# Kernel optimization log

Hardware: AMD Instinct MI355X
Metric: run time of the kernel (lower is better)

Reference implementation:

```python
import jax, jax.numpy as jnp
import numpy as np

D = 256  # out_size / d_model
B, S = 8, 4096


def setup_inputs() -> dict:
    key = jax.random.key(0)
    ks = jax.random.split(key, 10)
    std = 1.0 / np.sqrt(D)
    x = jax.random.normal(ks[0], (B, S, D), dtype=jnp.float32)
    Wq = jax.random.uniform(ks[1], (D, D), jnp.float32, -std, std)
    bq = jax.random.uniform(ks[2], (D,), jnp.float32, -std, std)
    Wk = jax.random.uniform(ks[3], (D, D), jnp.float32, -std, std)
    bk = jax.random.uniform(ks[4], (D,), jnp.float32, -std, std)
    Wv = jax.random.uniform(ks[5], (D, D), jnp.float32, -std, std)
    bv = jax.random.uniform(ks[6], (D,), jnp.float32, -std, std)
    Wo = jax.random.uniform(ks[7], (D, D), jnp.float32, -std, std)
    bo = jax.random.uniform(ks[8], (D,), jnp.float32, -std, std)
    cv = jax.random.normal(ks[9], (D, 1), dtype=jnp.float32)
    return {"x": x, "Wq": Wq, "bq": bq, "Wk": Wk, "bk": bk,
            "Wv": Wv, "bv": bv, "Wo": Wo, "bo": bo, "cv": cv}


def reference(x, Wq, bq, Wk, bk, Wv, bv, Wo, bo, cv):
    # Local single-head attention: separate matmul / softmax / matmul
    q = jnp.einsum('bsd,de->bse', x, Wq) + bq
    k = jnp.einsum('bsd,de->bse', x, Wk) + bk
    v = jnp.einsum('bsd,de->bse', x, Wv) + bv
    scale = jnp.sqrt(jnp.asarray(D, dtype=x.dtype))
    scores = jnp.einsum('bqd,bkd->bqk', q, k) / scale  # [B,S,S]
    attn = jax.nn.softmax(scores, axis=-1)
    ctx = jnp.einsum('bqk,bkd->bqd', attn, v)
    logits = jnp.einsum('bsd,de->bse', ctx, Wo) + bo
    # Global context-vector pooling weights (softmax over sequence dim)
    w = jnp.einsum('bsd,dk->bsk', logits, cv)          # [B,S,1]
    nw = jax.nn.softmax(w, axis=1)
    return logits * nw
```

## Files before the change

### kernel.cpp

```cpp
#include <hip/hip_runtime.h>
#include <math.h>
#include <cstddef>
#include <cstdint>

#define B_ 8
#define S_ 4096
#define D_ 256

typedef __attribute__((ext_vector_type(8))) short short8v;
typedef __attribute__((ext_vector_type(4))) short short4v;
typedef __attribute__((ext_vector_type(4))) float float4v;

__device__ __forceinline__ unsigned short f2bf(float f) {
  unsigned u = __float_as_uint(f);
  return (unsigned short)((u + 0x7FFF + ((u >> 16) & 1)) >> 16);
}
__device__ __forceinline__ float bf2f(unsigned short h) {
  return __uint_as_float((unsigned)h << 16);
}
__device__ __forceinline__ unsigned packp(float p) {
  const unsigned short hh = f2bf(p);
  const unsigned short ll = f2bf(p - bf2f(hh));
  return ((unsigned)hh << 16) | (unsigned)ll;
}

__global__ __launch_bounds__(256) void wsplit_kernel(
    const float* __restrict__ Wq, const float* __restrict__ Wk,
    const float* __restrict__ Wv, const float* __restrict__ Wo,
    short* __restrict__ wsp) {
  const int mat = blockIdx.x >> 4;
  const int k0  = (blockIdx.x & 15) << 4;
  const float* W = (mat == 0) ? Wq : (mat == 1) ? Wk : (mat == 2) ? Wv : Wo;
  const int n = threadIdx.x;
  short8v h0, h1, l0, l1;
#pragma unroll
  for (int j = 0; j < 8; ++j) {
    float y = W[(size_t)(k0 + j) * 256 + n];
    unsigned short hh = f2bf(y);
    h0[j] = (short)hh; l0[j] = (short)f2bf(y - bf2f(hh));
    y = W[(size_t)(k0 + 8 + j) * 256 + n];
    hh = f2bf(y);
    h1[j] = (short)hh; l1[j] = (short)f2bf(y - bf2f(hh));
  }
  short* dh = wsp + (size_t)mat * 131072 + (size_t)n * 256 + k0;
  short* dl = dh + 65536;
  *(short8v*)(dh + 0) = h0; *(short8v*)(dh + 8) = h1;
  *(short8v*)(dl + 0) = l0; *(short8v*)(dl + 8) = l1;
}

__global__ __launch_bounds__(512, 2) void proj_qkv_mfma(
    const float* __restrict__ x, const short* __restrict__ wsp,
    const float* __restrict__ bq, const float* __restrict__ bk,
    const float* __restrict__ bvv,
    short* __restrict__ qh, short* __restrict__ ql,
    short* __restrict__ kh, short* __restrict__ kl,
    short* __restrict__ vth, short* __restrict__ vtl) {
  __shared__ __align__(16) short sWh[256 * 40];
  __shared__ __align__(16) short sWl[256 * 40];

  const int t    = threadIdx.x;
  const int w    = t >> 6;
  const int lane = t & 63;
  const int m    = lane & 15;
  const int quad = lane >> 4;
  const size_t r0 = (size_t)blockIdx.x * 128;
  const size_t srow = r0 + 16 * w + m;

  short8v xh[8], xl[8];
#pragma unroll
  for (int kk = 0; kk < 8; ++kk) {
    const float* xp = x + srow * 256 + kk * 32 + quad * 8;
    const float4 a = *(const float4*)xp;
    const float4 b2 = *(const float4*)(xp + 4);
    const float v[8] = {a.x, a.y, a.z, a.w, b2.x, b2.y, b2.z, b2.w};
    short8v h, l;
#pragma unroll
    for (int e = 0; e < 8; ++e) {
      const unsigned short hh = f2bf(v[e]);
      h[e] = (short)hh; l[e] = (short)f2bf(v[e] - bf2f(hh));
    }
    xh[kk] = h; xl[kk] = l;
  }

  const int nr   = t >> 1;
  const int kh16 = (t & 1) << 4;
  short8v rh0, rh1, rl0, rl1;
  {
    const short* gh = wsp + (size_t)nr * 256 + kh16;
    const short* gl = gh + 65536;
    rh0 = *(const short8v*)gh;       rh1 = *(const short8v*)(gh + 8);
    rl0 = *(const short8v*)gl;       rl1 = *(const short8v*)(gl + 8);
  }

#pragma unroll
  for (int p = 0; p < 3; ++p) {
    float4v acc[16];
#pragma unroll
    for (int nt = 0; nt < 16; ++nt) acc[nt] = (float4v){0.f, 0.f, 0.f, 0.f};

    for (int kk = 0; kk < 8; ++kk) {
      asm volatile("s_waitcnt lgkmcnt(0)" ::: "memory");
      __builtin_amdgcn_s_barrier();
      asm volatile("" ::: "memory");
      *(short8v*)&sWh[nr * 40 + kh16]     = rh0;
      *(short8v*)&sWh[nr * 40 + kh16 + 8] = rh1;
      *(short8v*)&sWl[nr * 40 + kh16]     = rl0;
      *(short8v*)&sWl[nr * 40 + kh16 + 8] = rl1;
      {
        const int np = (kk < 7) ? p : p + 1;
        const int nk = (kk < 7) ? kk + 1 : 0;
        if (np < 3) {
          const short* gh = wsp + (size_t)np * 131072 +
                            (size_t)nr * 256 + nk * 32 + kh16;
          const short* gl = gh + 65536;
          rh0 = *(const short8v*)gh;   rh1 = *(const short8v*)(gh + 8);
          rl0 = *(const short8v*)gl;   rl1 = *(const short8v*)(gl + 8);
        }
      }
      asm volatile("s_waitcnt lgkmcnt(0)" ::: "memory");
      __builtin_amdgcn_s_barrier();
      asm volatile("" ::: "memory");

      __builtin_amdgcn_s_setprio(1);
#pragma unroll
      for (int nt = 0; nt < 16; ++nt) {
        const short8v wh = *(const short8v*)&sWh[(nt * 16 + m) * 40 + quad * 8];
        const short8v wl = *(const short8v*)&sWl[(nt * 16 + m) * 40 + quad * 8];
        if (p < 2) {
          acc[nt] = __builtin_amdgcn_mfma_f32_16x16x32_bf16(wh, xh[kk], acc[nt], 0, 0, 0);
          acc[nt] = __builtin_amdgcn_mfma_f32_16x16x32_bf16(wh, xl[kk], acc[nt], 0, 0, 0);
          acc[nt] = __builtin_amdgcn_mfma_f32_16x16x32_bf16(wl, xh[kk], acc[nt], 0, 0, 0);
        } else {
          acc[nt] = __builtin_amdgcn_mfma_f32_16x16x32_bf16(xh[kk], wh, acc[nt], 0, 0, 0);
          acc[nt] = __builtin_amdgcn_mfma_f32_16x16x32_bf16(xh[kk], wl, acc[nt], 0, 0, 0);
          acc[nt] = __builtin_amdgcn_mfma_f32_16x16x32_bf16(xl[kk], wh, acc[nt], 0, 0, 0);
        }
      }
      __builtin_amdgcn_s_setprio(0);
    }

    if (p < 2) {
      const float scale = (p == 0) ? 0.0625f : 1.0f;
      short* oh = (p == 0) ? qh : kh;
      short* ol = (p == 0) ? ql : kl;
      const float* bias = (p == 0) ? bq : bk;
#pragma unroll
      for (int nt = 0; nt < 16; ++nt) {
        const float4 bb = *(const float4*)(bias + nt * 16 + quad * 4);
        const float bb4[4] = {bb.x, bb.y, bb.z, bb.w};
        short4v h4, l4;
#pragma unroll
        for (int r = 0; r < 4; ++r) {
          const float y = (acc[nt][r] + bb4[r]) * scale;
          const unsigned short hh = f2bf(y);
          h4[r] = (short)hh; l4[r] = (short)f2bf(y - bf2f(hh));
        }
        *(short4v*)(oh + srow * 256 + nt * 16 + quad * 4) = h4;
        *(short4v*)(ol + srow * 256 + nt * 16 + quad * 4) = l4;
      }
    } else {
      const int bidx = (int)(r0 >> 12);
      const size_t bD = (size_t)bidx * (D_ * (size_t)S_);
      const int sl0 = (int)(r0 & 4095) + 16 * w + quad * 4;
#pragma unroll
      for (int nt = 0; nt < 16; ++nt) {
        const int d = nt * 16 + m;
        const float bn = bvv[d];
        short4v h4, l4;
#pragma unroll
        for (int r = 0; r < 4; ++r) {
          const float y = acc[nt][r] + bn;
          const unsigned short hh = f2bf(y);
          h4[r] = (short)hh; l4[r] = (short)f2bf(y - bf2f(hh));
        }
        *(short4v*)(vth + bD + (size_t)d * S_ + sl0) = h4;
        *(short4v*)(vtl + bD + (size_t)d * S_ + sl0) = l4;
      }
    }
  }
}

__global__ __launch_bounds__(512, 2) void gemm_out_mfma(
    const float* __restrict__ ctx, const short* __restrict__ wsp,
    const float* __restrict__ bo, const float* __restrict__ cv,
    float* __restrict__ out, float* __restrict__ wvec) {
  __shared__ __align__(16) short sWh[256 * 40];
  __shared__ __align__(16) short sWl[256 * 40];

  const int t    = threadIdx.x;
  const int w    = t >> 6;
  const int lane = t & 63;
  const int m    = lane & 15;
  const int quad = lane >> 4;
  const size_t r0 = (size_t)blockIdx.x * 128;
  const size_t srow = r0 + 16 * w + m;
  const short* wbase = wsp + (size_t)3 * 131072;

  short8v ah[8], al[8];
#pragma unroll
  for (int kk = 0; kk < 8; ++kk) {
    const float* xp = ctx + srow * 256 + kk * 32 + quad * 8;
    const float4 a = *(const float4*)xp;
    const float4 b2 = *(const float4*)(xp + 4);
    const float v[8] = {a.x, a.y, a.z, a.w, b2.x, b2.y, b2.z, b2.w};
    short8v h, l;
#pragma unroll
    for (int e = 0; e < 8; ++e) {
      const unsigned short hh = f2bf(v[e]);
      h[e] = (short)hh; l[e] = (short)f2bf(v[e] - bf2f(hh));
    }
    ah[kk] = h; al[kk] = l;
  }

  const int nr   = t >> 1;
  const int kh16 = (t & 1) << 4;
  short8v rh0, rh1, rl0, rl1;
  {
    const short* gh = wbase + (size_t)nr * 256 + kh16;
    const short* gl = gh + 65536;
    rh0 = *(const short8v*)gh;       rh1 = *(const short8v*)(gh + 8);
    rl0 = *(const short8v*)gl;       rl1 = *(const short8v*)(gl + 8);
  }

  float4v acc[16];
#pragma unroll
  for (int nt = 0; nt < 16; ++nt) acc[nt] = (float4v){0.f, 0.f, 0.f, 0.f};

  for (int kk = 0; kk < 8; ++kk) {
    asm volatile("s_waitcnt lgkmcnt(0)" ::: "memory");
    __builtin_amdgcn_s_barrier();
    asm volatile("" ::: "memory");
    *(short8v*)&sWh[nr * 40 + kh16]     = rh0;
    *(short8v*)&sWh[nr * 40 + kh16 + 8] = rh1;
    *(short8v*)&sWl[nr * 40 + kh16]     = rl0;
    *(short8v*)&sWl[nr * 40 + kh16 + 8] = rl1;
    if (kk < 7) {
      const short* gh = wbase + (size_t)nr * 256 + (kk + 1) * 32 + kh16;
      const short* gl = gh + 65536;
      rh0 = *(const short8v*)gh;   rh1 = *(const short8v*)(gh + 8);
      rl0 = *(const short8v*)gl;   rl1 = *(const short8v*)(gl + 8);
    }
    asm volatile("s_waitcnt lgkmcnt(0)" ::: "memory");
    __builtin_amdgcn_s_barrier();
    asm volatile("" ::: "memory");

    __builtin_amdgcn_s_setprio(1);
#pragma unroll
    for (int nt = 0; nt < 16; ++nt) {
      const short8v wh = *(const short8v*)&sWh[(nt * 16 + m) * 40 + quad * 8];
      const short8v wl = *(const short8v*)&sWl[(nt * 16 + m) * 40 + quad * 8];
      acc[nt] = __builtin_amdgcn_mfma_f32_16x16x32_bf16(wh, ah[kk], acc[nt], 0, 0, 0);
      acc[nt] = __builtin_amdgcn_mfma_f32_16x16x32_bf16(wh, al[kk], acc[nt], 0, 0, 0);
      acc[nt] = __builtin_amdgcn_mfma_f32_16x16x32_bf16(wl, ah[kk], acc[nt], 0, 0, 0);
    }
    __builtin_amdgcn_s_setprio(0);
  }

  float wp = 0.f;
  float* orow = out + srow * 256;
#pragma unroll
  for (int nt = 0; nt < 16; ++nt) {
    const float4 bb = *(const float4*)(bo + nt * 16 + quad * 4);
    const float4 cc = *(const float4*)(cv + nt * 16 + quad * 4);
    float4 o;
    o.x = acc[nt][0] + bb.x; o.y = acc[nt][1] + bb.y;
    o.z = acc[nt][2] + bb.z; o.w = acc[nt][3] + bb.w;
    wp += o.x * cc.x + o.y * cc.y + o.z * cc.z + o.w * cc.w;
    *(float4*)(orow + nt * 16 + quad * 4) = o;
  }
  wp += __shfl_xor(wp, 16, 64);
  wp += __shfl_xor(wp, 32, 64);
  if (quad == 0) wvec[srow] = wp;
}

__global__ __launch_bounds__(512, 2) void flash_attn_mfma(
    const short* __restrict__ qh, const short* __restrict__ ql,
    const short* __restrict__ kh, const short* __restrict__ kl,
    const short* __restrict__ vth, const short* __restrict__ vtl,
    float* __restrict__ ctx) {
  __shared__ __align__(16) short sK[16896];
  __shared__ __align__(16) short sV[20480];
  __shared__ __align__(16) unsigned int sP[8][16][36];
  __shared__ __align__(16) float sAlpha[8][16];
  __shared__ __align__(16) int sF[8];
  __shared__ __align__(16) float sL[128];

  const int t    = threadIdx.x;
  const int w    = t >> 6;
  const int lane = t & 63;
  const int m    = lane & 15;
  const int quad = lane >> 4;
  const int q0   = blockIdx.x * 128;
  const int b    = blockIdx.y;
  const size_t sd = (size_t)b * (S_ * (size_t)D_);
  const size_t bD = (size_t)b * (D_ * (size_t)S_);

  short8v aqh[8], aql[8];
  {
    const size_t row = sd + (size_t)(q0 + 16 * w + m) * D_;
#pragma unroll
    for (int kk = 0; kk < 8; ++kk) {
      const size_t off = row + kk * 32 + quad * 8;
      aqh[kk] = *(const short8v*)(qh + off);
      aql[kk] = *(const short8v*)(ql + off);
    }
  }

  short8v ones;
#pragma unroll
  for (int e = 0; e < 8; ++e) ones[e] = (short)0x3F80;

  float4v acc[8][2];
#pragma unroll
  for (int qt = 0; qt < 8; ++qt) {
    acc[qt][0] = (float4v){0.f, 0.f, 0.f, 0.f};
    acc[qt][1] = (float4v){0.f, 0.f, 0.f, 0.f};
  }
  float4v accl = (float4v){0.f, 0.f, 0.f, 0.f};
  float m_i = -INFINITY;

  const int kr0 = t >> 5;
  const int kc0 = (t & 31) << 3;
  const int vd  = t >> 1;
  const int vjh = (t & 1) << 4;

  short8v rKh0, rKh1, rKl0, rKl1;
  short8v rVh0, rVh1, rVl0, rVl1;

  {
    const size_t g0 = sd + (size_t)kr0 * D_ + kc0;
    const size_t g1 = sd + (size_t)(16 + kr0) * D_ + kc0;
    rKh0 = *(const short8v*)(kh + g0);
    rKh1 = *(const short8v*)(kh + g1);
    rKl0 = *(const short8v*)(kl + g0);
    rKl1 = *(const short8v*)(kl + g1);
  }

  for (int jt = 0; jt < 128; ++jt) {
    const int j0 = jt << 5;

    *(short8v*)&sK[kr0 * 264 + kc0]               = rKh0;
    *(short8v*)&sK[(16 + kr0) * 264 + kc0]        = rKh1;
    *(short8v*)&sK[8448 + kr0 * 264 + kc0]        = rKl0;
    *(short8v*)&sK[8448 + (16 + kr0) * 264 + kc0] = rKl1;
    {
      const size_t g = bD + (size_t)vd * S_ + j0 + vjh;
      rVh0 = *(const short8v*)(vth + g);
      rVh1 = *(const short8v*)(vth + g + 8);
      rVl0 = *(const short8v*)(vtl + g);
      rVl1 = *(const short8v*)(vtl + g + 8);
    }
    asm volatile("s_waitcnt lgkmcnt(0)" ::: "memory");
    __builtin_amdgcn_s_barrier();
    asm volatile("" ::: "memory");

    float4v s0 = (float4v){0.f, 0.f, 0.f, 0.f};
    float4v s1 = (float4v){0.f, 0.f, 0.f, 0.f};
    __builtin_amdgcn_s_setprio(1);
#pragma unroll
    for (int kk = 0; kk < 8; ++kk) {
      const int co = kk * 32 + quad * 8;
      const short8v bh0 = *(const short8v*)&sK[m * 264 + co];
      const short8v bl0 = *(const short8v*)&sK[8448 + m * 264 + co];
      const short8v bh1 = *(const short8v*)&sK[(16 + m) * 264 + co];
      const short8v bl1 = *(const short8v*)&sK[8448 + (16 + m) * 264 + co];
      s0 = __builtin_amdgcn_mfma_f32_16x16x32_bf16(bh0, aqh[kk], s0, 0, 0, 0);
      s0 = __builtin_amdgcn_mfma_f32_16x16x32_bf16(bh0, aql[kk], s0, 0, 0, 0);
      s0 = __builtin_amdgcn_mfma_f32_16x16x32_bf16(bl0, aqh[kk], s0, 0, 0, 0);
      s1 = __builtin_amdgcn_mfma_f32_16x16x32_bf16(bh1, aqh[kk], s1, 0, 0, 0);
      s1 = __builtin_amdgcn_mfma_f32_16x16x32_bf16(bh1, aql[kk], s1, 0, 0, 0);
      s1 = __builtin_amdgcn_mfma_f32_16x16x32_bf16(bl1, aqh[kk], s1, 0, 0, 0);
    }
    __builtin_amdgcn_s_setprio(0);

    float alpha_p = 1.0f;
    int fired = 0;
    {
      float mx = fmaxf(fmaxf(fmaxf(s0[0], s0[1]), fmaxf(s0[2], s0[3])),
                       fmaxf(fmaxf(s1[0], s1[1]), fmaxf(s1[2], s1[3])));
      mx = fmaxf(mx, __shfl_xor(mx, 16, 64));
      mx = fmaxf(mx, __shfl_xor(mx, 32, 64));
      if (__any(mx > m_i + 8.0f)) {
        const float mnew = fmaxf(m_i, mx);
        alpha_p = __expf(m_i - mnew);
        m_i = mnew;
        fired = 1;
        float al[4];
#pragma unroll
        for (int r = 0; r < 4; ++r) al[r] = __shfl(alpha_p, 20 * quad + r, 64);
#pragma unroll
        for (int r = 0; r < 4; ++r) accl[r] *= al[r];
      }
    }
    if (quad == 0) sAlpha[w][m] = alpha_p;
    if (lane == 0) sF[w] = fired;

    {
      uint4 w0, w1;
      w0.x = packp(__expf(s0[0] - m_i));
      w0.y = packp(__expf(s0[1] - m_i));
      w0.z = packp(__expf(s0[2] - m_i));
      w0.w = packp(__expf(s0[3] - m_i));
      w1.x = packp(__expf(s1[0] - m_i));
      w1.y = packp(__expf(s1[1] - m_i));
      w1.z = packp(__expf(s1[2] - m_i));
      w1.w = packp(__expf(s1[3] - m_i));
      *(uint4*)&sP[w][m][4 * quad]      = w0;
      *(uint4*)&sP[w][m][16 + 4 * quad] = w1;
    }

    *(short8v*)&sV[vd * 40 + vjh]               = rVh0;
    *(short8v*)&sV[vd * 40 + vjh + 8]           = rVh1;
    *(short8v*)&sV[10240 + vd * 40 + vjh]       = rVl0;
    *(short8v*)&sV[10240 + vd * 40 + vjh + 8]   = rVl1;
    if (jt < 127) {
      const int j0n = j0 + 32;
      const size_t g0 = sd + (size_t)(j0n + kr0) * D_ + kc0;
      const size_t g1 = sd + (size_t)(j0n + 16 + kr0) * D_ + kc0;
      rKh0 = *(const short8v*)(kh + g0);
      rKh1 = *(const short8v*)(kh + g1);
      rKl0 = *(const short8v*)(kl + g0);
      rKl1 = *(const short8v*)(kl + g1);
    }
    asm volatile("s_waitcnt lgkmcnt(0)" ::: "memory");
    __builtin_amdgcn_s_barrier();
    asm volatile("" ::: "memory");

    {
      const uint4 f0 = *(const uint4*)&sF[0];
      const uint4 f1 = *(const uint4*)&sF[4];
      if (f0.x | f0.y | f0.z | f0.w | f1.x | f1.y | f1.z | f1.w) {
#pragma unroll
        for (int qt = 0; qt < 8; ++qt) {
          const float4 alf = *(const float4*)&sAlpha[qt][quad << 2];
          const float a4[4] = {alf.x, alf.y, alf.z, alf.w};
#pragma unroll
          for (int r = 0; r < 4; ++r) {
            acc[qt][0][r] *= a4[r];
            acc[qt][1][r] *= a4[r];
          }
        }
      }
    }

    __builtin_amdgcn_s_setprio(1);
    {
      const int vr0 = ((w << 1) * 16 + m) * 40 + quad * 8;
      const short8v bh0 = *(const short8v*)&sV[vr0];
      const short8v bl0 = *(const short8v*)&sV[10240 + vr0];
      const short8v bh1 = *(const short8v*)&sV[vr0 + 640];
      const short8v bl1 = *(const short8v*)&sV[10240 + vr0 + 640];
#pragma unroll
      for (int qt = 0; qt < 8; ++qt) {
        short8v ph, pl;
        {
          const uint4 pa = *(const uint4*)&sP[qt][m][quad * 8];
          const uint4 pb = *(const uint4*)&sP[qt][m][quad * 8 + 4];
          ph[0] = (short)(pa.x >> 16); pl[0] = (short)(pa.x & 0xffff);
          ph[1] = (short)(pa.y >> 16); pl[1] = (short)(pa.y & 0xffff);
          ph[2] = (short)(pa.z >> 16); pl[2] = (short)(pa.z & 0xffff);
          ph[3] = (short)(pa.w >> 16); pl[3] = (short)(pa.w & 0xffff);
          ph[4] = (short)(pb.x >> 16); pl[4] = (short)(pb.x & 0xffff);
          ph[5] = (short)(pb.y >> 16); pl[5] = (short)(pb.y & 0xffff);
          ph[6] = (short)(pb.z >> 16); pl[6] = (short)(pb.z & 0xffff);
          ph[7] = (short)(pb.w >> 16); pl[7] = (short)(pb.w & 0xffff);
        }
        if (qt == w) {
          accl = __builtin_amdgcn_mfma_f32_16x16x32_bf16(ph, ones, accl, 0, 0, 0);
          accl = __builtin_amdgcn_mfma_f32_16x16x32_bf16(pl, ones, accl, 0, 0, 0);
        }
        acc[qt][0] = __builtin_amdgcn_mfma_f32_16x16x32_bf16(ph, bh0, acc[qt][0], 0, 0, 0);
        acc[qt][0] = __builtin_amdgcn_mfma_f32_16x16x32_bf16(ph, bl0, acc[qt][0], 0, 0, 0);
        acc[qt][0] = __builtin_amdgcn_mfma_f32_16x16x32_bf16(pl, bh0, acc[qt][0], 0, 0, 0);
        acc[qt][1] = __builtin_amdgcn_mfma_f32_16x16x32_bf16(ph, bh1, acc[qt][1], 0, 0, 0);
        acc[qt][1] = __builtin_amdgcn_mfma_f32_16x16x32_bf16(ph, bl1, acc[qt][1], 0, 0, 0);
        acc[qt][1] = __builtin_amdgcn_mfma_f32_16x16x32_bf16(pl, bh1, acc[qt][1], 0, 0, 0);
      }
    }
    __builtin_amdgcn_s_setprio(0);
  }

  if (m == 0) {
#pragma unroll
    for (int r = 0; r < 4; ++r) sL[16 * w + 4 * quad + r] = accl[r];
  }
  __syncthreads();
#pragma unroll
  for (int qt = 0; qt < 8; ++qt) {
    const float4 lf = *(const float4*)&sL[16 * qt + (quad << 2)];
    const float inv4[4] = {1.0f / lf.x, 1.0f / lf.y, 1.0f / lf.z, 1.0f / lf.w};
#pragma unroll
    for (int dtl = 0; dtl < 2; ++dtl) {
      const int d = ((w << 1) + dtl) * 16 + m;
#pragma unroll
      for (int r = 0; r < 4; ++r) {
        ctx[sd + (size_t)(q0 + 16 * qt + 4 * quad + r) * D_ + d] =
            acc[qt][dtl][r] * inv4[r];
      }
    }
  }
}

__global__ __launch_bounds__(256) void softmax_scale_kernel(
    float* __restrict__ out, const float* __restrict__ wv) {
  __shared__ float red[4];
  const int t = threadIdx.x;
  const int wave = t >> 6, lane = t & 63;
  const int b = blockIdx.x >> 8;
  const float* wb = wv + (size_t)b * S_;

  float mx = -INFINITY;
#pragma unroll
  for (int i = 0; i < 16; ++i) mx = fmaxf(mx, wb[t + (i << 8)]);
#pragma unroll
  for (int off = 32; off > 0; off >>= 1) mx = fmaxf(mx, __shfl_xor(mx, off, 64));
  if (lane == 0) red[wave] = mx;
  __syncthreads();
  const float M = fmaxf(fmaxf(red[0], red[1]), fmaxf(red[2], red[3]));
  float sum = 0.f;
#pragma unroll
  for (int i = 0; i < 16; ++i) sum += __expf(wb[t + (i << 8)] - M);
#pragma unroll
  for (int off = 32; off > 0; off >>= 1) sum += __shfl_xor(sum, off, 64);
  __syncthreads();
  if (lane == 0) red[wave] = sum;
  __syncthreads();
  const float inv = 1.0f / (red[0] + red[1] + red[2] + red[3]);

  float4* o4 = (float4*)out;
  const size_t g0 = (size_t)blockIdx.x * 1024 + t;
#pragma unroll
  for (int i = 0; i < 4; ++i) {
    const size_t g = g0 + (size_t)(i << 8);
    const float sc = __expf(wv[g >> 6] - M) * inv;
    float4 vv = o4[g];
    vv.x *= sc; vv.y *= sc; vv.z *= sc; vv.w *= sc;
    o4[g] = vv;
  }
}

extern "C" void kernel_launch(void* const* d_in, const int* in_sizes, int n_in,
                              void* d_out, int out_size, void* d_ws, size_t ws_size,
                              hipStream_t stream) {
  const float* x  = (const float*)d_in[0];
  const float* Wq = (const float*)d_in[1];
  const float* bq = (const float*)d_in[2];
  const float* Wk = (const float*)d_in[3];
  const float* bk = (const float*)d_in[4];
  const float* Wv = (const float*)d_in[5];
  const float* bv = (const float*)d_in[6];
  const float* Wo = (const float*)d_in[7];
  const float* bo = (const float*)d_in[8];
  const float* cv = (const float*)d_in[9];
  float* out = (float*)d_out;

  const size_t N = (size_t)B_ * S_ * D_;
  short* qh  = (short*)d_ws;
  short* ql  = qh + N;
  short* kh  = ql + N;
  short* kl  = kh + N;
  short* vth = kl + N;
  short* vtl = vth + N;
  float* ctx = (float*)(vtl + N);
  float* w   = ctx + N;
  short* wsp = (short*)(w + (size_t)B_ * S_);

  wsplit_kernel<<<64, 256, 0, stream>>>(Wq, Wk, Wv, Wo, wsp);
  proj_qkv_mfma<<<256, 512, 0, stream>>>(x, wsp, bq, bk, bv,
                                         qh, ql, kh, kl, vth, vtl);
  flash_attn_mfma<<<dim3(32, 8), 512, 0, stream>>>(qh, ql, kh, kl, vth, vtl, ctx);
  gemm_out_mfma<<<256, 512, 0, stream>>>(ctx, wsp, bo, cv, out, w);
  softmax_scale_kernel<<<2048, 256, 0, stream>>>(out, w);
}
```

Before: 578.3 us.

## Load V fragments directly from global into registers and split P hi/lo LDS buffers

Each wave now reads its V^T MFMA operand fragments straight from global memory into registers, prefetched one tile ahead, instead of staging V through shared memory. The packed hi/lo P buffer is replaced by separate bf16 hi and lo arrays, so the PV loop loads ready-made short8 operands without unpacking. This removes the V LDS writes and reads and the unpack ALU work, and lowers LDS footprint. In exchange each wave issues its own narrower global loads, which may be less coalesced, and the data comes from cache rather than shared staging.

```diff
diff --git a/kernel.cpp b/kernel.cpp
--- a/kernel.cpp
+++ b/kernel.cpp
@@ -17,11 +17,6 @@
 }
 __device__ __forceinline__ float bf2f(unsigned short h) {
   return __uint_as_float((unsigned)h << 16);
-}
-__device__ __forceinline__ unsigned packp(float p) {
-  const unsigned short hh = f2bf(p);
-  const unsigned short ll = f2bf(p - bf2f(hh));
-  return ((unsigned)hh << 16) | (unsigned)ll;
 }
 
 __global__ __launch_bounds__(256) void wsplit_kernel(
@@ -279,8 +274,8 @@
     const short* __restrict__ vth, const short* __restrict__ vtl,
     float* __restrict__ ctx) {
   __shared__ __align__(16) short sK[16896];
-  __shared__ __align__(16) short sV[20480];
-  __shared__ __align__(16) unsigned int sP[8][16][36];
+  __shared__ __align__(16) short sPh[8][16][40];
+  __shared__ __align__(16) short sPl[8][16][40];
   __shared__ __align__(16) float sAlpha[8][16];
   __shared__ __align__(16) int sF[8];
   __shared__ __align__(16) float sL[128];
@@ -321,11 +316,14 @@
 
   const int kr0 = t >> 5;
   const int kc0 = (t & 31) << 3;
-  const int vd  = t >> 1;
-  const int vjh = (t & 1) << 4;
+
+  const short* vg0h = vth + bD + (size_t)(((w << 1) + 0) * 16 + m) * S_ + quad * 8;
+  const short* vg0l = vtl + bD + (size_t)(((w << 1) + 0) * 16 + m) * S_ + quad * 8;
+  const short* vg1h = vth + bD + (size_t)(((w << 1) + 1) * 16 + m) * S_ + quad * 8;
+  const short* vg1l = vtl + bD + (size_t)(((w << 1) + 1) * 16 + m) * S_ + quad * 8;
 
   short8v rKh0, rKh1, rKl0, rKl1;
-  short8v rVh0, rVh1, rVl0, rVl1;
+  short8v rVh0, rVl0, rVh1, rVl1;
 
   {
     const size_t g0 = sd + (size_t)kr0 * D_ + kc0;
@@ -334,6 +332,10 @@
     rKh1 = *(const short8v*)(kh + g1);
     rKl0 = *(const short8v*)(kl + g0);
     rKl1 = *(const short8v*)(kl + g1);
+    rVh0 = *(const short8v*)vg0h;
+    rVl0 = *(const short8v*)vg0l;
+    rVh1 = *(const short8v*)vg1h;
+    rVl1 = *(const short8v*)vg1l;
   }
 
   for (int jt = 0; jt < 128; ++jt) {
@@ -343,13 +345,6 @@
     *(short8v*)&sK[(16 + kr0) * 264 + kc0]        = rKh1;
     *(short8v*)&sK[8448 + kr0 * 264 + kc0]        = rKl0;
     *(short8v*)&sK[8448 + (16 + kr0) * 264 + kc0] = rKl1;
-    {
-      const size_t g = bD + (size_t)vd * S_ + j0 + vjh;
-      rVh0 = *(const short8v*)(vth + g);
-      rVh1 = *(const short8v*)(vth + g + 8);
-      rVl0 = *(const short8v*)(vtl + g);
-      rVl1 = *(const short8v*)(vtl + g + 8);
-    }
     asm volatile("s_waitcnt lgkmcnt(0)" ::: "memory");
     __builtin_amdgcn_s_barrier();
     asm volatile("" ::: "memory");
@@ -396,23 +391,22 @@
     if (lane == 0) sF[w] = fired;
 
     {
-      uint4 w0, w1;
-      w0.x = packp(__expf(s0[0] - m_i));
-      w0.y = packp(__expf(s0[1] - m_i));
-      w0.z = packp(__expf(s0[2] - m_i));
-      w0.w = packp(__expf(s0[3] - m_i));
-      w1.x = packp(__expf(s1[0] - m_i));
-      w1.y = packp(__expf(s1[1] - m_i));
-      w1.z = packp(__expf(s1[2] - m_i));
-      w1.w = packp(__expf(s1[3] - m_i));
-      *(uint4*)&sP[w][m][4 * quad]      = w0;
-      *(uint4*)&sP[w][m][16 + 4 * quad] = w1;
-    }
-
-    *(short8v*)&sV[vd * 40 + vjh]               = rVh0;
-    *(short8v*)&sV[vd * 40 + vjh + 8]           = rVh1;
-    *(short8v*)&sV[10240 + vd * 40 + vjh]       = rVl0;
-    *(short8v*)&sV[10240 + vd * 40 + vjh + 8]   = rVl1;
+      short4v h4a, l4a, h4b, l4b;
+#pragma unroll
+      for (int r = 0; r < 4; ++r) {
+        const float pA = __expf(s0[r] - m_i);
+        const unsigned short hA = f2bf(pA);
+        h4a[r] = (short)hA; l4a[r] = (short)f2bf(pA - bf2f(hA));
+        const float pB = __expf(s1[r] - m_i);
+        const unsigned short hB = f2bf(pB);
+        h4b[r] = (short)hB; l4b[r] = (short)f2bf(pB - bf2f(hB));
+      }
+      *(short4v*)&sPh[w][m][4 * quad]      = h4a;
+      *(short4v*)&sPh[w][m][16 + 4 * quad] = h4b;
+      *(short4v*)&sPl[w][m][4 * quad]      = l4a;
+      *(short4v*)&sPl[w][m][16 + 4 * quad] = l4b;
+    }
+
     if (jt < 127) {
       const int j0n = j0 + 32;
       const size_t g0 = sd + (size_t)(j0n + kr0) * D_ + kc0;
@@ -444,40 +438,30 @@
     }
 
     __builtin_amdgcn_s_setprio(1);
-    {
-      const int vr0 = ((w << 1) * 16 + m) * 40 + quad * 8;
-      const short8v bh0 = *(const short8v*)&sV[vr0];
-      const short8v bl0 = *(const short8v*)&sV[10240 + vr0];
-      const short8v bh1 = *(const short8v*)&sV[vr0 + 640];
-      const short8v bl1 = *(const short8v*)&sV[10240 + vr0 + 640];
-#pragma unroll
-      for (int qt = 0; qt < 8; ++qt) {
-        short8v ph, pl;
-        {
-          const uint4 pa = *(const uint4*)&sP[qt][m][quad * 8];
-          const uint4 pb = *(const uint4*)&sP[qt][m][quad * 8 + 4];
-          ph[0] = (short)(pa.x >> 16); pl[0] = (short)(pa.x & 0xffff);
-          ph[1] = (short)(pa.y >> 16); pl[1] = (short)(pa.y & 0xffff);
-          ph[2] = (short)(pa.z >> 16); pl[2] = (short)(pa.z & 0xffff);
-          ph[3] = (short)(pa.w >> 16); pl[3] = (short)(pa.w & 0xffff);
-          ph[4] = (short)(pb.x >> 16); pl[4] = (short)(pb.x & 0xffff);
-          ph[5] = (short)(pb.y >> 16); pl[5] = (short)(pb.y & 0xffff);
-          ph[6] = (short)(pb.z >> 16); pl[6] = (short)(pb.z & 0xffff);
-          ph[7] = (short)(pb.w >> 16); pl[7] = (short)(pb.w & 0xffff);
-        }
-        if (qt == w) {
-          accl = __builtin_amdgcn_mfma_f32_16x16x32_bf16(ph, ones, accl, 0, 0, 0);
-          accl = __builtin_amdgcn_mfma_f32_16x16x32_bf16(pl, ones, accl, 0, 0, 0);
-        }
-        acc[qt][0] = __builtin_amdgcn_mfma_f32_16x16x32_bf16(ph, bh0, acc[qt][0], 0, 0, 0);
-        acc[qt][0] = __builtin_amdgcn_mfma_f32_16x16x32_bf16(ph, bl0, acc[qt][0], 0, 0, 0);
-        acc[qt][0] = __builtin_amdgcn_mfma_f32_16x16x32_bf16(pl, bh0, acc[qt][0], 0, 0, 0);
-        acc[qt][1] = __builtin_amdgcn_mfma_f32_16x16x32_bf16(ph, bh1, acc[qt][1], 0, 0, 0);
-        acc[qt][1] = __builtin_amdgcn_mfma_f32_16x16x32_bf16(ph, bl1, acc[qt][1], 0, 0, 0);
-        acc[qt][1] = __builtin_amdgcn_mfma_f32_16x16x32_bf16(pl, bh1, acc[qt][1], 0, 0, 0);
-      }
+#pragma unroll
+    for (int qt = 0; qt < 8; ++qt) {
+      const short8v ph = *(const short8v*)&sPh[qt][m][quad * 8];
+      const short8v pl = *(const short8v*)&sPl[qt][m][quad * 8];
+      if (qt == w) {
+        accl = __builtin_amdgcn_mfma_f32_16x16x32_bf16(ph, ones, accl, 0, 0, 0);
+        accl = __builtin_amdgcn_mfma_f32_16x16x32_bf16(pl, ones, accl, 0, 0, 0);
+      }
+      acc[qt][0] = __builtin_amdgcn_mfma_f32_16x16x32_bf16(ph, rVh0, acc[qt][0], 0, 0, 0);
+      acc[qt][0] = __builtin_amdgcn_mfma_f32_16x16x32_bf16(ph, rVl0, acc[qt][0], 0, 0, 0);
+      acc[qt][0] = __builtin_amdgcn_mfma_f32_16x16x32_bf16(pl, rVh0, acc[qt][0], 0, 0, 0);
+      acc[qt][1] = __builtin_amdgcn_mfma_f32_16x16x32_bf16(ph, rVh1, acc[qt][1], 0, 0, 0);
+      acc[qt][1] = __builtin_amdgcn_mfma_f32_16x16x32_bf16(ph, rVl1, acc[qt][1], 0, 0, 0);
+      acc[qt][1] = __builtin_amdgcn_mfma_f32_16x16x32_bf16(pl, rVh1, acc[qt][1], 0, 0, 0);
     }
     __builtin_amdgcn_s_setprio(0);
+
+    if (jt < 127) {
+      const int j0n = j0 + 32;
+      rVh0 = *(const short8v*)(vg0h + j0n);
+      rVl0 = *(const short8v*)(vg0l + j0n);
+      rVh1 = *(const short8v*)(vg1h + j0n);
+      rVl1 = *(const short8v*)(vg1l + j0n);
+    }
   }
 
   if (m == 0) {
```

Measured after the change: 550.0 us. 1.05x faster.
